# Performance work log

Hardware: AMD Instinct MI355X
Metric: run time of the kernel (lower is better)

Reference implementation:

```python
import jax, jax.numpy as jnp
import numpy as np

DIM = 768
HEADS = 12
HEAD_DIM = DIM // HEADS
SCALE = HEAD_DIM ** -0.5
LN_EPS = 1e-5


def setup_inputs() -> dict:
    key = jax.random.key(0)
    ks = jax.random.split(key, 12)
    B, N, C = 8, 1024, DIM
    g = (6.0 / (C + 3 * C)) ** 0.5  # xavier_uniform bound for qkv
    gp = (6.0 / (C + C)) ** 0.5     # xavier_uniform bound for proj
    return {
        "x": jax.random.normal(ks[0], (B, N, C), jnp.float32),
        "w_qkv_id": jax.random.uniform(ks[1], (3 * C, C), jnp.float32, -g, g),
        "w_qkv_cloth": jax.random.uniform(ks[2], (3 * C, C), jnp.float32, -g, g),
        "w_proj_id": jax.random.uniform(ks[3], (C, C), jnp.float32, -gp, gp),
        "b_proj_id": jnp.zeros((C,), jnp.float32),
        "w_proj_cloth": jax.random.uniform(ks[4], (C, C), jnp.float32, -gp, gp),
        "b_proj_cloth": jnp.zeros((C,), jnp.float32),
        "ln_id_w": jnp.ones((C,), jnp.float32),
        "ln_id_b": jnp.zeros((C,), jnp.float32),
        "ln_cloth_w": jnp.ones((C,), jnp.float32),
        "ln_cloth_b": jnp.zeros((C,), jnp.float32),
        "orth_scale": jnp.asarray(0.1, jnp.float32),
    }


def _layernorm(x, w, b):
    mu = jnp.mean(x, axis=-1, keepdims=True)
    var = jnp.var(x, axis=-1, keepdims=True)
    return (x - mu) * jax.lax.rsqrt(var + LN_EPS) * w + b


def _split_heads(qkv, B, N):
    qkv = qkv.reshape(B, N, 3, HEADS, HEAD_DIM).transpose(2, 0, 3, 1, 4)
    return qkv[0], qkv[1], qkv[2]


def _attn(q, k, v):
    s = jnp.einsum("bhnd,bhmd->bhnm", q, k) * SCALE
    s = jnp.clip(s, -20.0, 20.0)
    a = jax.nn.softmax(s, axis=-1)
    a = jnp.where(jnp.isnan(a), jnp.zeros_like(a), a)  # nan guard (dropout = eval/identity)
    return jnp.einsum("bhnm,bhmd->bhnd", a, v)


def reference(x, w_qkv_id, w_qkv_cloth, w_proj_id, b_proj_id, w_proj_cloth,
              b_proj_cloth, ln_id_w, ln_id_b, ln_cloth_w, ln_cloth_b, orth_scale):
    B, N, C = x.shape
    q_id, k_id, v_id = _split_heads(x @ w_qkv_id.T, B, N)
    q_cl, k_cl, v_cl = _split_heads(x @ w_qkv_cloth.T, B, N)

    # Gram-Schmidt orthogonal projection of q_id against q_cloth
    dot = jnp.sum(q_id * q_cl, axis=-1, keepdims=True)          # [B,H,N,1]
    norm_sq = jnp.sum(q_cl * q_cl, axis=-1, keepdims=True) + 1e-5
    coeff = jnp.clip(dot / norm_sq, -1.0, 1.0)
    scale = jnp.clip(orth_scale, 0.0, 1.0)
    q_id_ortho = q_id - scale * (coeff * q_cl)
    saliency = jnp.clip(jnp.mean(jnp.abs(dot) / jnp.sqrt(norm_sq), axis=1), 0.0, 1.0)  # [B,N,1]

    out_id = _attn(q_id_ortho, k_id, v_id).transpose(0, 2, 1, 3).reshape(B, N, C)
    out_cl = _attn(q_cl, k_cl, v_cl).transpose(0, 2, 1, 3).reshape(B, N, C)

    id_feat = _layernorm(out_id @ w_proj_id.T + b_proj_id, ln_id_w, ln_id_b)
    cl_feat = _layernorm(out_cl @ w_proj_cloth.T + b_proj_cloth, ln_cloth_w, ln_cloth_b)
    return id_feat, cl_feat, saliency
```

## Files before the change

kernel.cpp:

```cpp
#include <hip/hip_runtime.h>

typedef unsigned short u16;
typedef short s16x8 __attribute__((ext_vector_type(8)));
typedef float f32x4 __attribute__((ext_vector_type(4)));

#define DEV __device__ __forceinline__

#if __has_builtin(__builtin_amdgcn_exp2f)
#define EXP2F(x) __builtin_amdgcn_exp2f(x)
#else
#define EXP2F(x) exp2f(x)
#endif

DEV u16 f2bf(float f) {
  unsigned int u = __float_as_uint(f);
  u = (u + 0x7fffu + ((u >> 16) & 1u)) >> 16;
  return (u16)u;
}
DEV float bf2f(u16 h) { return __uint_as_float(((unsigned int)h) << 16); }
DEV unsigned int pk_trunc(float lo, float hi) {
  return __builtin_amdgcn_perm(__float_as_uint(hi), __float_as_uint(lo), 0x07060302u);
}

DEV void g2l16(const void* g, void* l) {
  __builtin_amdgcn_global_load_lds(
      (const __attribute__((address_space(1))) unsigned int*)g,
      (__attribute__((address_space(3))) unsigned int*)l, 16, 0, 0);
}

#define SPLANE 6291456

__global__ __launch_bounds__(256) void k_cvt(const float* __restrict__ x,
                                             const float* __restrict__ wqi,
                                             const float* __restrict__ wqc,
                                             const float* __restrict__ wpi,
                                             const float* __restrict__ wpc,
                                             u16* __restrict__ xb,
                                             u16* __restrict__ wqkv,
                                             u16* __restrict__ wproj) {
  int i = blockIdx.x * 256 + threadIdx.x;
  const float* src; u16* dst; int off;
  if (i < 1572864)      { src = x;   dst = xb;             off = 0; }
  else if (i < 2015232) { src = wqi; dst = wqkv;           off = 1572864; }
  else if (i < 2457600) { src = wqc; dst = wqkv + 1769472; off = 2015232; }
  else if (i < 2605056) { src = wpi; dst = wproj;          off = 2457600; }
  else                  { src = wpc; dst = wproj + 589824; off = 2605056; }
  int j = i - off;
  float4 v = ((const float4*)src)[j];
  ushort4 o;
  o.x = f2bf(v.x); o.y = f2bf(v.y); o.z = f2bf(v.z); o.w = f2bf(v.w);
  ((ushort4*)dst)[j] = o;
}

__global__ __launch_bounds__(256) void k_qkv_gemm(const u16* __restrict__ X,
                                                  const u16* __restrict__ Wq,
                                                  u16* __restrict__ QK,
                                                  u16* __restrict__ VT) {
  __shared__ __align__(16) u16 sm[18432];
  u16* lA = sm;
  u16* lB = sm + 8192;
  const int z = blockIdx.z;
  const int n0 = blockIdx.x * 128, m0 = blockIdx.y * 128;
  const u16* W = Wq + (size_t)z * 2304 * 768;
  const int tid = threadIdx.x;
  const int wave = tid >> 6, lane = tid & 63;
  const int wr = (wave >> 1) * 64, wc = (wave & 1) * 64;
  const int fr = lane & 15, fq = lane >> 4;

  f32x4 acc[4][4];
#pragma unroll
  for (int i = 0; i < 4; i++)
#pragma unroll
    for (int j = 0; j < 4; j++) acc[i][j] = (f32x4){0.f, 0.f, 0.f, 0.f};

  const int srow = lane >> 3;
  const int scol = ((lane & 7) ^ srow) * 8;

  for (int k0 = 0; k0 < 768; k0 += 64) {
    __syncthreads();
#pragma unroll
    for (int it = 0; it < 4; ++it) {
      int rb = wave * 32 + it * 8;
      g2l16(X + (size_t)(m0 + rb + srow) * 768 + k0 + scol, &lA[rb * 64]);
      g2l16(W + (size_t)(n0 + rb + srow) * 768 + k0 + scol, &lB[rb * 64]);
    }
    __syncthreads();
#pragma unroll
    for (int ks = 0; ks < 2; ++ks) {
      s16x8 af[4], bfr[4];
#pragma unroll
      for (int i = 0; i < 4; i++) {
        int row = wc + i * 16 + fr;
        af[i] = *(const s16x8*)&lB[row * 64 + (((ks * 4 + fq) ^ (row & 7)) * 8)];
      }
#pragma unroll
      for (int j = 0; j < 4; j++) {
        int row = wr + j * 16 + fr;
        bfr[j] = *(const s16x8*)&lA[row * 64 + (((ks * 4 + fq) ^ (row & 7)) * 8)];
      }
#pragma unroll
      for (int i = 0; i < 4; i++)
#pragma unroll
        for (int j = 0; j < 4; j++)
          acc[i][j] = __builtin_amdgcn_mfma_f32_16x16x32_bf16(af[i], bfr[j], acc[i][j], 0, 0, 0);
    }
  }

  __syncthreads();
  u16* ep = sm + wave * 4608;
#pragma unroll
  for (int i = 0; i < 4; i++)
#pragma unroll
    for (int j = 0; j < 4; j++) {
      unsigned int lo = (unsigned int)f2bf(acc[i][j][0]) | ((unsigned int)f2bf(acc[i][j][1]) << 16);
      unsigned int hi = (unsigned int)f2bf(acc[i][j][2]) | ((unsigned int)f2bf(acc[i][j][3]) << 16);
      uint2 pk; pk.x = lo; pk.y = hi;
      *(uint2*)&ep[(j * 16 + fr) * 72 + i * 16 + fq * 4] = pk;
    }
  __builtin_amdgcn_s_waitcnt(0);

  const int c0 = n0 + wc;
  const int t0 = m0 + wr;
  const int b = t0 >> 10, tt0 = t0 & 1023;
  if (c0 < 1536) {
    const int three = (c0 >= 768) ? 1 : 0;
    const int h = (c0 - three * 768) >> 6;
    u16* dst = QK + ((size_t)z * 2 + three) * SPLANE +
               ((size_t)(b * 12 + h) * 1024 + tt0) * 64;
#pragma unroll
    for (int pass = 0; pass < 8; ++pass) {
      int row = pass * 8 + (lane >> 3);
      int dch = (lane & 7) * 8;
      *(uint4*)&dst[(size_t)row * 64 + dch] = *(const uint4*)&ep[row * 72 + dch];
    }
  } else {
    const int h = (c0 - 1536) >> 6;
    u16* dst = VT + (size_t)z * SPLANE + ((size_t)(b * 12 + h) * 64) * 1024 + tt0;
#pragma unroll
    for (int pass = 0; pass < 8; ++pass) {
      int d = pass * 8 + (lane >> 3);
      int tch = (lane & 7) * 8;
      unsigned int w0[4];
#pragma unroll
      for (int k2 = 0; k2 < 4; k2++) {
        unsigned int lo = ep[(tch + k2 * 2) * 72 + d];
        unsigned int hi = ep[(tch + k2 * 2 + 1) * 72 + d];
        w0[k2] = lo | (hi << 16);
      }
      uint4 val;
      val.x = w0[0]; val.y = w0[1]; val.z = w0[2]; val.w = w0[3];
      *(uint4*)&dst[(size_t)d * 1024 + tch] = val;
    }
  }
}

__global__ __launch_bounds__(256) void k_ortho(u16* __restrict__ QK,
                                               const float* __restrict__ orth_scale,
                                               float* __restrict__ sal) {
  const int wave = threadIdx.x >> 6, lane = threadIdx.x & 63;
  const int row = blockIdx.x * 4 + wave;
  const int b = row >> 10, n = row & 1023;
  const float scale = fminf(fmaxf(orth_scale[0], 0.f), 1.f);
  u16* qid = QK;
  u16* qcl = QK + (size_t)2 * SPLANE;
  float sacc = 0.f;
  for (int h = 0; h < 12; ++h) {
    size_t off = (((size_t)(b * 12 + h)) * 1024 + n) * 64 + lane;
    float qi = bf2f(qid[off]);
    float qc = bf2f(qcl[off]);
    float d = qi * qc, nq = qc * qc;
#pragma unroll
    for (int s = 1; s < 64; s <<= 1) { d += __shfl_xor(d, s); nq += __shfl_xor(nq, s); }
    nq += 1e-5f;
    float coeff = fminf(fmaxf(d / nq, -1.f), 1.f);
    qid[off] = f2bf(qi - scale * coeff * qc);
    sacc += fabsf(d) / sqrtf(nq);
  }
  if (lane == 0) sal[row] = fminf(fmaxf(sacc * (1.f / 12.f), 0.f), 1.f);
}

#define AST 72
#define PST 40
__global__ __launch_bounds__(256, 3) void k_attn(const u16* __restrict__ QK,
                                                 const u16* __restrict__ VT,
                                                 u16* __restrict__ aout) {
  __shared__ __align__(16) u16 sm[19456];
  u16* lK = sm;
  u16* lVT = sm + 4608;
  const int z = blockIdx.z, bh = blockIdx.y;
  const int q0 = blockIdx.x * 256;
  const int b = bh / 12, hd = bh - b * 12;
  const size_t plane = (size_t)bh * 65536;
  const u16* Q  = QK + (size_t)z * 2 * SPLANE + plane;
  const u16* K  = QK + ((size_t)z * 2 + 1) * SPLANE + plane;
  const u16* Vt = VT + (size_t)z * SPLANE + plane;

  const int tid = threadIdx.x, wave = tid >> 6, lane = tid & 63;
  const int fr = lane & 15, fq = lane >> 4;
  u16* lP = sm + 9216 + wave * 2560;

  s16x8 qf[4][2];
#pragma unroll
  for (int s = 0; s < 4; s++) {
    const u16* qrow = Q + (size_t)(q0 + wave * 64 + s * 16 + fr) * 64;
    qf[s][0] = *(const s16x8*)&qrow[fq * 8];
    qf[s][1] = *(const s16x8*)&qrow[32 + fq * 8];
  }

  f32x4 oacc[4][4];
  float lsum[4];
#pragma unroll
  for (int s = 0; s < 4; s++) {
    lsum[s] = 0.f;
#pragma unroll
    for (int j = 0; j < 4; j++) oacc[s][j] = (f32x4){0.f, 0.f, 0.f, 0.f};
  }

  const int srow = tid >> 3, sc8 = (tid & 7) * 8;

  uint4 rk0 = *(const uint4*)&K[(size_t)srow * 64 + sc8];
  uint4 rk1 = *(const uint4*)&K[(size_t)(srow + 32) * 64 + sc8];
  uint4 rv0 = *(const uint4*)&Vt[(size_t)srow * 1024 + sc8];
  uint4 rv1 = *(const uint4*)&Vt[(size_t)(srow + 32) * 1024 + sc8];

  for (int kv0 = 0; kv0 < 1024; kv0 += 64) {
    __syncthreads();
    *(uint4*)&lK[srow * AST + sc8]         = rk0;
    *(uint4*)&lK[(srow + 32) * AST + sc8]  = rk1;
    *(uint4*)&lVT[srow * AST + sc8]        = rv0;
    *(uint4*)&lVT[(srow + 32) * AST + sc8] = rv1;
    __syncthreads();

    {
      int nxt = (kv0 + 64) & 1023;
      const u16* kb = K + (size_t)nxt * 64;
      rk0 = *(const uint4*)&kb[(size_t)srow * 64 + sc8];
      rk1 = *(const uint4*)&kb[(size_t)(srow + 32) * 64 + sc8];
      const u16* vb = Vt + nxt;
      rv0 = *(const uint4*)&vb[(size_t)srow * 1024 + sc8];
      rv1 = *(const uint4*)&vb[(size_t)(srow + 32) * 1024 + sc8];
    }

#pragma unroll
    for (int ph = 0; ph < 2; ++ph) {
#pragma unroll
      for (int jh = 0; jh < 2; ++jh) {
        const int jt = ph * 2 + jh;
        s16x8 kf0 = *(const s16x8*)&lK[(jt * 16 + fr) * AST + fq * 8];
        s16x8 kf1 = *(const s16x8*)&lK[(jt * 16 + fr) * AST + 32 + fq * 8];
#pragma unroll
        for (int s = 0; s < 4; s++) {
          f32x4 t = (f32x4){0.f, 0.f, 0.f, 0.f};
          t = __builtin_amdgcn_mfma_f32_16x16x32_bf16(kf0, qf[s][0], t, 0, 0, 0);
          t = __builtin_amdgcn_mfma_f32_16x16x32_bf16(kf1, qf[s][1], t, 0, 0, 0);
          float p0 = EXP2F(fmaf(t[0], 0.18033688f, -28.8539008f));
          float p1 = EXP2F(fmaf(t[1], 0.18033688f, -28.8539008f));
          float p2 = EXP2F(fmaf(t[2], 0.18033688f, -28.8539008f));
          float p3 = EXP2F(fmaf(t[3], 0.18033688f, -28.8539008f));
          lsum[s] += (p0 + p1) + (p2 + p3);
          uint2 pk; pk.x = pk_trunc(p0, p1); pk.y = pk_trunc(p2, p3);
          *(uint2*)&lP[(s * 16 + fr) * PST + jh * 16 + fq * 4] = pk;
        }
      }
      __builtin_amdgcn_s_waitcnt(0);
      s16x8 pa[4];
#pragma unroll
      for (int s = 0; s < 4; s++) pa[s] = *(const s16x8*)&lP[(s * 16 + fr) * PST + fq * 8];
#pragma unroll
      for (int jt = 0; jt < 4; jt++) {
        s16x8 vb = *(const s16x8*)&lVT[(jt * 16 + fr) * AST + ph * 32 + fq * 8];
#pragma unroll
        for (int s = 0; s < 4; s++)
          oacc[s][jt] = __builtin_amdgcn_mfma_f32_16x16x32_bf16(pa[s], vb, oacc[s][jt], 0, 0, 0);
      }
    }
  }

#pragma unroll
  for (int s = 0; s < 4; s++) {
    float v = lsum[s];
    v += __shfl_xor(v, 16);
    v += __shfl_xor(v, 32);
    lsum[s] = v;
  }
#pragma unroll
  for (int s = 0; s < 4; s++) {
#pragma unroll
    for (int r = 0; r < 4; r++) {
      float inv = 1.f / __shfl(lsum[s], fq * 4 + r);
      int t = q0 + wave * 64 + s * 16 + fq * 4 + r;
      size_t base = ((size_t)z * 8192 + b * 1024 + t) * 768 + hd * 64 + fr;
#pragma unroll
      for (int jt = 0; jt < 4; jt++)
        aout[base + jt * 16] = f2bf(oacc[s][jt][r] * inv);
    }
  }
}

__global__ __launch_bounds__(256) void k_proj_gemm(const u16* __restrict__ A,
                                                   const u16* __restrict__ Wp,
                                                   const float* __restrict__ bias_id,
                                                   const float* __restrict__ bias_cl,
                                                   u16* __restrict__ out) {
  __shared__ __align__(16) u16 sm[18432];
  u16* lA = sm;
  u16* lB = sm + 8192;
  const int z = blockIdx.z;
  const int n0 = blockIdx.x * 128, m0 = blockIdx.y * 128;
  const u16* Az = A + (size_t)z * 8192 * 768;
  const u16* Wz = Wp + (size_t)z * 768 * 768;
  const float* bias = z ? bias_cl : bias_id;
  u16* oz = out + (size_t)z * 8192 * 768;
  const int tid = threadIdx.x;
  const int wave = tid >> 6, lane = tid & 63;
  const int wr = (wave >> 1) * 64, wc = (wave & 1) * 64;
  const int fr = lane & 15, fq = lane >> 4;

  float bv[4][4];
#pragma unroll
  for (int i = 0; i < 4; i++)
#pragma unroll
    for (int r = 0; r < 4; r++) bv[i][r] = bias[n0 + wc + i * 16 + fq * 4 + r];

  f32x4 acc[4][4];
#pragma unroll
  for (int i = 0; i < 4; i++)
#pragma unroll
    for (int j = 0; j < 4; j++) acc[i][j] = (f32x4){0.f, 0.f, 0.f, 0.f};

  const int srow = lane >> 3;
  const int scol = ((lane & 7) ^ srow) * 8;

  for (int k0 = 0; k0 < 768; k0 += 64) {
    __syncthreads();
#pragma unroll
    for (int it = 0; it < 4; ++it) {
      int rb = wave * 32 + it * 8;
      g2l16(Az + (size_t)(m0 + rb + srow) * 768 + k0 + scol, &lA[rb * 64]);
      g2l16(Wz + (size_t)(n0 + rb + srow) * 768 + k0 + scol, &lB[rb * 64]);
    }
    __syncthreads();
#pragma unroll
    for (int ks = 0; ks < 2; ++ks) {
      s16x8 af[4], bfr[4];
#pragma unroll
      for (int i = 0; i < 4; i++) {
        int row = wc + i * 16 + fr;
        af[i] = *(const s16x8*)&lB[row * 64 + (((ks * 4 + fq) ^ (row & 7)) * 8)];
      }
#pragma unroll
      for (int j = 0; j < 4; j++) {
        int row = wr + j * 16 + fr;
        bfr[j] = *(const s16x8*)&lA[row * 64 + (((ks * 4 + fq) ^ (row & 7)) * 8)];
      }
#pragma unroll
      for (int i = 0; i < 4; i++)
#pragma unroll
        for (int j = 0; j < 4; j++)
          acc[i][j] = __builtin_amdgcn_mfma_f32_16x16x32_bf16(af[i], bfr[j], acc[i][j], 0, 0, 0);
    }
  }

  __syncthreads();
  u16* ep = sm + wave * 4608;
#pragma unroll
  for (int i = 0; i < 4; i++)
#pragma unroll
    for (int j = 0; j < 4; j++) {
      unsigned int lo = (unsigned int)f2bf(acc[i][j][0] + bv[i][0]) |
                        ((unsigned int)f2bf(acc[i][j][1] + bv[i][1]) << 16);
      unsigned int hi = (unsigned int)f2bf(acc[i][j][2] + bv[i][2]) |
                        ((unsigned int)f2bf(acc[i][j][3] + bv[i][3]) << 16);
      uint2 pk; pk.x = lo; pk.y = hi;
      *(uint2*)&ep[(j * 16 + fr) * 72 + i * 16 + fq * 4] = pk;
    }
  __builtin_amdgcn_s_waitcnt(0);

  const int c0 = n0 + wc;
#pragma unroll
  for (int pass = 0; pass < 8; ++pass) {
    int row = pass * 8 + (lane >> 3);
    int dch = (lane & 7) * 8;
    u16* dst = oz + (size_t)(m0 + wr + row) * 768 + c0;
    *(uint4*)&dst[dch] = *(const uint4*)&ep[row * 72 + dch];
  }
}

__global__ __launch_bounds__(256) void k_ln(const u16* __restrict__ pin,
                                            const float* __restrict__ w_id,
                                            const float* __restrict__ b_id,
                                            const float* __restrict__ w_cl,
                                            const float* __restrict__ b_cl,
                                            float* __restrict__ out) {
  __shared__ float red[2][8];
  const int row = blockIdx.x;
  const int z = row >> 13;
  const float* w = z ? w_cl : w_id;
  const float* bb = z ? b_cl : b_id;
  const u16* x = pin + (size_t)row * 768;
  float v[3];
  float s = 0.f, s2 = 0.f;
#pragma unroll
  for (int i = 0; i < 3; i++) {
    v[i] = bf2f(x[threadIdx.x + i * 256]);
    s += v[i];
    s2 += v[i] * v[i];
  }
#pragma unroll
  for (int sh = 1; sh < 64; sh <<= 1) { s += __shfl_xor(s, sh); s2 += __shfl_xor(s2, sh); }
  const int wave = threadIdx.x >> 6, lane = threadIdx.x & 63;
  if (lane == 0) { red[0][wave] = s; red[1][wave] = s2; }
  __syncthreads();
  s = red[0][0] + red[0][1] + red[0][2] + red[0][3];
  s2 = red[1][0] + red[1][1] + red[1][2] + red[1][3];
  float mu = s * (1.f / 768.f);
  float var = s2 * (1.f / 768.f) - mu * mu;
  float rstd = rsqrtf(fmaxf(var, 0.f) + 1e-5f);
  float* o = out + (size_t)row * 768;
#pragma unroll
  for (int i = 0; i < 3; i++) {
    int c = threadIdx.x + i * 256;
    o[c] = (v[i] - mu) * rstd * w[c] + bb[c];
  }
}

extern "C" void kernel_launch(void* const* d_in, const int* in_sizes, int n_in,
                              void* d_out, int out_size, void* d_ws, size_t ws_size,
                              hipStream_t stream) {
  const float* x        = (const float*)d_in[0];
  const float* w_qkv_id = (const float*)d_in[1];
  const float* w_qkv_cl = (const float*)d_in[2];
  const float* w_proj_id= (const float*)d_in[3];
  const float* b_proj_id= (const float*)d_in[4];
  const float* w_proj_cl= (const float*)d_in[5];
  const float* b_proj_cl= (const float*)d_in[6];
  const float* ln_id_w  = (const float*)d_in[7];
  const float* ln_id_b  = (const float*)d_in[8];
  const float* ln_cl_w  = (const float*)d_in[9];
  const float* ln_cl_b  = (const float*)d_in[10];
  const float* orth     = (const float*)d_in[11];
  float* out = (float*)d_out;

  u16* xb    = (u16*)d_ws;
  u16* wqkv  = xb + 6291456;
  u16* wproj = wqkv + 3538944;
  u16* qk    = wproj + 1179648;
  u16* vt    = qk + 25165824;
  u16* aout  = vt + 12582912;
  u16* pout  = qk;

  k_cvt<<<10752, 256, 0, stream>>>(x, w_qkv_id, w_qkv_cl, w_proj_id, w_proj_cl,
                                   xb, wqkv, wproj);
  k_qkv_gemm<<<dim3(18, 64, 2), 256, 0, stream>>>(xb, wqkv, qk, vt);
  k_ortho<<<2048, 256, 0, stream>>>(qk, orth, out + 12582912);
  k_attn<<<dim3(4, 96, 2), 256, 0, stream>>>(qk, vt, aout);
  k_proj_gemm<<<dim3(6, 64, 2), 256, 0, stream>>>(aout, wproj, b_proj_id, b_proj_cl, pout);
  k_ln<<<16384, 256, 0, stream>>>(pout, ln_id_w, ln_id_b, ln_cl_w, ln_cl_b, out);
}
```

Before: 323.4 us.

## Rewrite QKV GEMM as 256x256 double-buffered pipelined kernel with block swizzle

Replaces the 128x128, 4-wave QKV GEMM with a 256x256-tile, 8-wave kernel that double-buffers LDS and interleaves global-to-LDS slab loads with MFMA quarters under explicit barriers, vmcnt waits and priority bumps. A 1D grid with an XCD-aware swizzle improves L2 reuse across blocks. The intent is to overlap memory traffic with matrix compute and raise arithmetic intensity per block. It uses 128KB of LDS and more registers, and the hand-tuned wait counts and barriers are fragile.

```diff
diff --git a/kernel.cpp b/kernel.cpp
--- a/kernel.cpp
+++ b/kernel.cpp
@@ -52,105 +52,189 @@
   ((ushort4*)dst)[j] = o;
 }
 
-__global__ __launch_bounds__(256) void k_qkv_gemm(const u16* __restrict__ X,
-                                                  const u16* __restrict__ Wq,
-                                                  u16* __restrict__ QK,
-                                                  u16* __restrict__ VT) {
-  __shared__ __align__(16) u16 sm[18432];
-  u16* lA = sm;
-  u16* lB = sm + 8192;
-  const int z = blockIdx.z;
-  const int n0 = blockIdx.x * 128, m0 = blockIdx.y * 128;
-  const u16* W = Wq + (size_t)z * 2304 * 768;
+
+#define BAR __builtin_amdgcn_s_barrier()
+#define WAIT_LGKM0 asm volatile("s_waitcnt lgkmcnt(0)" ::: "memory")
+#define WAIT_VM(n) asm volatile("s_waitcnt vmcnt(" #n ")" ::: "memory")
+#define PRIO1 __builtin_amdgcn_s_setprio(1)
+#define PRIO0 __builtin_amdgcn_s_setprio(0)
+
+#define SLAB(gbase, rowoff, kt, ldst) \
+  g2l16((gbase) + (size_t)((rowoff) + wrow) * 768 + (kt) * 64 + csrc, (ldst) + wave * 512)
+
+template<int I0>
+DEV void ldA2(s16x8 (&dst)[2][2], const u16* bw, int aOff, int c0, int c1) {
+#pragma unroll
+  for (int i = 0; i < 2; i++) {
+    dst[i][0] = *(const s16x8*)&bw[aOff + (I0 + i) * 1024 + c0];
+    dst[i][1] = *(const s16x8*)&bw[aOff + (I0 + i) * 1024 + c1];
+  }
+}
+template<int J0>
+DEV void ldB4(s16x8 (&dst)[4][2], const u16* bx, int bOff, int c0, int c1) {
+#pragma unroll
+  for (int j = 0; j < 4; j++) {
+    dst[j][0] = *(const s16x8*)&bx[bOff + (J0 + j) * 1024 + c0];
+    dst[j][1] = *(const s16x8*)&bx[bOff + (J0 + j) * 1024 + c1];
+  }
+}
+template<int I0, int J0>
+DEV void mmq(const s16x8 (&af)[2][2], const s16x8 (&bf)[4][2], f32x4 (&acc)[4][8]) {
+#pragma unroll
+  for (int ks = 0; ks < 2; ks++)
+#pragma unroll
+    for (int i = 0; i < 2; i++)
+#pragma unroll
+      for (int j = 0; j < 4; j++)
+        acc[I0 + i][J0 + j] = __builtin_amdgcn_mfma_f32_16x16x32_bf16(
+            af[i][ks], bf[j][ks], acc[I0 + i][J0 + j], 0, 0, 0);
+}
+
+__global__ __launch_bounds__(512, 2) void k_qkv_gemm(const u16* __restrict__ X,
+                                                     const u16* __restrict__ Wq,
+                                                     u16* __restrict__ QK,
+                                                     u16* __restrict__ VT) {
+  __shared__ __align__(16) u16 sm[65536];
+
+  const int idx = blockIdx.x;
+  const int swz = (idx & 7) * 72 + (idx >> 3);
+  const int bx = swz % 9;
+  const int tmp = swz / 9;
+  const int by = tmp & 31;
+  const int z = tmp >> 5;
+  const int n0 = bx * 256, m0 = by * 256;
+
   const int tid = threadIdx.x;
   const int wave = tid >> 6, lane = tid & 63;
-  const int wr = (wave >> 1) * 64, wc = (wave & 1) * 64;
+  const int wr = wave >> 2, wc = wave & 3;
   const int fr = lane & 15, fq = lane >> 4;
 
-  f32x4 acc[4][4];
+  const int r8 = lane >> 3;
+  const int csrc = ((lane & 7) ^ r8) * 8;
+  const int wrow = wave * 8 + r8;
+
+  const int c0 = (fq ^ (fr & 7)) * 8;
+  const int c1 = ((fq + 4) ^ (fr & 7)) * 8;
+  const int aOff = (wc * 64 + fr) * 64;
+  const int bOff = (wr * 128 + fr) * 64;
+
+  const u16* GA = Wq + (size_t)z * (2304 * 768) + (size_t)n0 * 768;
+  const u16* GB = X + (size_t)m0 * 768;
+
+  u16* const lw0 = sm;
+  u16* const lx0 = sm + 16384;
+  u16* const lw1 = sm + 32768;
+  u16* const lx1 = sm + 49152;
+
+  f32x4 acc[4][8];
 #pragma unroll
   for (int i = 0; i < 4; i++)
 #pragma unroll
-    for (int j = 0; j < 4; j++) acc[i][j] = (f32x4){0.f, 0.f, 0.f, 0.f};
-
-  const int srow = lane >> 3;
-  const int scol = ((lane & 7) ^ srow) * 8;
-
-  for (int k0 = 0; k0 < 768; k0 += 64) {
-    __syncthreads();
-#pragma unroll
-    for (int it = 0; it < 4; ++it) {
-      int rb = wave * 32 + it * 8;
-      g2l16(X + (size_t)(m0 + rb + srow) * 768 + k0 + scol, &lA[rb * 64]);
-      g2l16(W + (size_t)(n0 + rb + srow) * 768 + k0 + scol, &lB[rb * 64]);
-    }
-    __syncthreads();
-#pragma unroll
-    for (int ks = 0; ks < 2; ++ks) {
-      s16x8 af[4], bfr[4];
-#pragma unroll
-      for (int i = 0; i < 4; i++) {
-        int row = wc + i * 16 + fr;
-        af[i] = *(const s16x8*)&lB[row * 64 + (((ks * 4 + fq) ^ (row & 7)) * 8)];
-      }
-#pragma unroll
-      for (int j = 0; j < 4; j++) {
-        int row = wr + j * 16 + fr;
-        bfr[j] = *(const s16x8*)&lA[row * 64 + (((ks * 4 + fq) ^ (row & 7)) * 8)];
-      }
-#pragma unroll
-      for (int i = 0; i < 4; i++)
-#pragma unroll
-        for (int j = 0; j < 4; j++)
-          acc[i][j] = __builtin_amdgcn_mfma_f32_16x16x32_bf16(af[i], bfr[j], acc[i][j], 0, 0, 0);
-    }
+    for (int j = 0; j < 8; j++) acc[i][j] = (f32x4){0.f, 0.f, 0.f, 0.f};
+
+  SLAB(GA,   0, 0, lw0);
+  SLAB(GA,  64, 0, lw0 + 4096);
+  SLAB(GA, 128, 0, lw0 + 8192);
+  SLAB(GA, 192, 0, lw0 + 12288);
+  SLAB(GB,   0, 0, lx0);
+  SLAB(GB,  64, 0, lx0 + 4096);
+  SLAB(GB, 128, 0, lx0 + 8192);
+  SLAB(GB, 192, 0, lx0 + 12288);
+  SLAB(GA,   0, 1, lw1);
+  SLAB(GA,  64, 1, lw1 + 4096);
+  WAIT_VM(2);
+  BAR;
+
+  s16x8 afA[2][2], afB[2][2], bfA[4][2], bfB[4][2];
+
+#pragma unroll
+  for (int it = 0; it < 6; ++it) {
+    const int ktB = 2 * it + 1;
+    const int ktN = 2 * it + 2;
+    const int ktM = 2 * it + 3;
+    const bool last = (it == 5);
+
+    ldA2<0>(afA, lw0, aOff, c0, c1);
+    ldB4<0>(bfA, lx0, bOff, c0, c1);
+    SLAB(GA, 128, ktB, lw1 + 8192);
+    SLAB(GA, 192, ktB, lw1 + 12288);
+    BAR; WAIT_LGKM0; PRIO1; mmq<0, 0>(afA, bfA, acc); PRIO0; BAR;
+    ldB4<4>(bfB, lx0, bOff, c0, c1);
+    SLAB(GB,   0, ktB, lx1);
+    SLAB(GB,  64, ktB, lx1 + 4096);
+    BAR; WAIT_LGKM0; PRIO1; mmq<0, 4>(afA, bfB, acc); PRIO0; BAR;
+    ldA2<2>(afB, lw0, aOff, c0, c1);
+    SLAB(GB, 128, ktB, lx1 + 8192);
+    SLAB(GB, 192, ktB, lx1 + 12288);
+    BAR; WAIT_LGKM0; PRIO1; mmq<2, 4>(afB, bfB, acc); PRIO0; BAR;
+    if (!last) { SLAB(GA, 0, ktN, lw0); SLAB(GA, 64, ktN, lw0 + 4096); }
+    BAR; PRIO1; mmq<2, 0>(afB, bfA, acc); PRIO0;
+    if (!last) { WAIT_VM(2); } else { WAIT_VM(0); }
+    BAR;
+    ldA2<0>(afA, lw1, aOff, c0, c1);
+    ldB4<0>(bfA, lx1, bOff, c0, c1);
+    if (!last) { SLAB(GA, 128, ktN, lw0 + 8192); SLAB(GA, 192, ktN, lw0 + 12288); }
+    BAR; WAIT_LGKM0; PRIO1; mmq<0, 0>(afA, bfA, acc); PRIO0; BAR;
+    ldB4<4>(bfB, lx1, bOff, c0, c1);
+    if (!last) { SLAB(GB, 0, ktN, lx0); SLAB(GB, 64, ktN, lx0 + 4096); }
+    BAR; WAIT_LGKM0; PRIO1; mmq<0, 4>(afA, bfB, acc); PRIO0; BAR;
+    ldA2<2>(afB, lw1, aOff, c0, c1);
+    if (!last) { SLAB(GB, 128, ktN, lx0 + 8192); SLAB(GB, 192, ktN, lx0 + 12288); }
+    BAR; WAIT_LGKM0; PRIO1; mmq<2, 4>(afB, bfB, acc); PRIO0; BAR;
+    if (!last) { SLAB(GA, 0, ktM, lw1); SLAB(GA, 64, ktM, lw1 + 4096); }
+    BAR; PRIO1; mmq<2, 0>(afB, bfA, acc); PRIO0;
+    if (!last) WAIT_VM(2);
+    BAR;
   }
 
   __syncthreads();
   u16* ep = sm + wave * 4608;
-#pragma unroll
-  for (int i = 0; i < 4; i++)
-#pragma unroll
-    for (int j = 0; j < 4; j++) {
-      unsigned int lo = (unsigned int)f2bf(acc[i][j][0]) | ((unsigned int)f2bf(acc[i][j][1]) << 16);
-      unsigned int hi = (unsigned int)f2bf(acc[i][j][2]) | ((unsigned int)f2bf(acc[i][j][3]) << 16);
-      uint2 pk; pk.x = lo; pk.y = hi;
-      *(uint2*)&ep[(j * 16 + fr) * 72 + i * 16 + fq * 4] = pk;
-    }
-  __builtin_amdgcn_s_waitcnt(0);
-
-  const int c0 = n0 + wc;
-  const int t0 = m0 + wr;
-  const int b = t0 >> 10, tt0 = t0 & 1023;
-  if (c0 < 1536) {
-    const int three = (c0 >= 768) ? 1 : 0;
-    const int h = (c0 - three * 768) >> 6;
-    u16* dst = QK + ((size_t)z * 2 + three) * SPLANE +
-               ((size_t)(b * 12 + h) * 1024 + tt0) * 64;
-#pragma unroll
-    for (int pass = 0; pass < 8; ++pass) {
-      int row = pass * 8 + (lane >> 3);
-      int dch = (lane & 7) * 8;
-      *(uint4*)&dst[(size_t)row * 64 + dch] = *(const uint4*)&ep[row * 72 + dch];
-    }
-  } else {
-    const int h = (c0 - 1536) >> 6;
-    u16* dst = VT + (size_t)z * SPLANE + ((size_t)(b * 12 + h) * 64) * 1024 + tt0;
-#pragma unroll
-    for (int pass = 0; pass < 8; ++pass) {
-      int d = pass * 8 + (lane >> 3);
-      int tch = (lane & 7) * 8;
-      unsigned int w0[4];
-#pragma unroll
-      for (int k2 = 0; k2 < 4; k2++) {
-        unsigned int lo = ep[(tch + k2 * 2) * 72 + d];
-        unsigned int hi = ep[(tch + k2 * 2 + 1) * 72 + d];
-        w0[k2] = lo | (hi << 16);
-      }
-      uint4 val;
-      val.x = w0[0]; val.y = w0[1]; val.z = w0[2]; val.w = w0[3];
-      *(uint4*)&dst[(size_t)d * 1024 + tch] = val;
-    }
+  const int c0h = n0 + wc * 64;
+  const int three = (c0h >= 1536) ? 2 : ((c0h >= 768) ? 1 : 0);
+  const int hh = (c0h - three * 768) >> 6;
+#pragma unroll
+  for (int jp = 0; jp < 2; ++jp) {
+#pragma unroll
+    for (int i = 0; i < 4; i++)
+#pragma unroll
+      for (int j4 = 0; j4 < 4; j4++) {
+        const int j = jp * 4 + j4;
+        uint2 pk;
+        pk.x = (unsigned int)f2bf(acc[i][j][0]) | ((unsigned int)f2bf(acc[i][j][1]) << 16);
+        pk.y = (unsigned int)f2bf(acc[i][j][2]) | ((unsigned int)f2bf(acc[i][j][3]) << 16);
+        *(uint2*)&ep[(j4 * 16 + fr) * 72 + i * 16 + fq * 4] = pk;
+      }
+    WAIT_LGKM0;
+    const int trow0 = m0 + wr * 128 + jp * 64;
+    const int b = trow0 >> 10, tt0 = trow0 & 1023;
+    if (three < 2) {
+      u16* dst = QK + ((size_t)z * 2 + three) * SPLANE +
+                 ((size_t)(b * 12 + hh) * 1024 + tt0) * 64;
+#pragma unroll
+      for (int pass = 0; pass < 8; ++pass) {
+        int row = pass * 8 + (lane >> 3);
+        int dch = (lane & 7) * 8;
+        *(uint4*)&dst[(size_t)row * 64 + dch] = *(const uint4*)&ep[row * 72 + dch];
+      }
+    } else {
+      u16* dst = VT + (size_t)z * SPLANE + ((size_t)(b * 12 + hh) * 64) * 1024 + tt0;
+#pragma unroll
+      for (int pass = 0; pass < 8; ++pass) {
+        int d = pass * 8 + (lane >> 3);
+        int tch = (lane & 7) * 8;
+        unsigned int w0[4];
+#pragma unroll
+        for (int k2 = 0; k2 < 4; k2++) {
+          unsigned int lo = ep[(tch + k2 * 2) * 72 + d];
+          unsigned int hi = ep[(tch + k2 * 2 + 1) * 72 + d];
+          w0[k2] = lo | (hi << 16);
+        }
+        uint4 val;
+        val.x = w0[0]; val.y = w0[1]; val.z = w0[2]; val.w = w0[3];
+        *(uint4*)&dst[(size_t)d * 1024 + tch] = val;
+      }
+    }
+    if (jp == 0) WAIT_LGKM0;
   }
 }
 
@@ -451,7 +535,7 @@
 
   k_cvt<<<10752, 256, 0, stream>>>(x, w_qkv_id, w_qkv_cl, w_proj_id, w_proj_cl,
                                    xb, wqkv, wproj);
-  k_qkv_gemm<<<dim3(18, 64, 2), 256, 0, stream>>>(xb, wqkv, qk, vt);
+  k_qkv_gemm<<<576, 512, 0, stream>>>(xb, wqkv, qk, vt);
   k_ortho<<<2048, 256, 0, stream>>>(qk, orth, out + 12582912);
   k_attn<<<dim3(4, 96, 2), 256, 0, stream>>>(qk, vt, aout);
   k_proj_gemm<<<dim3(6, 64, 2), 256, 0, stream>>>(aout, wproj, b_proj_id, b_proj_cl, pout);
```

After: 347.8 us. 1.08x slower.

## Double-buffer QKV GEMM LDS staging with vmcnt waits and block swizzle

Applied to the files above, without the earlier changes.

Restructures the QKV projection GEMM main loop to use two LDS buffers, so the global-to-LDS loads for the next K slice run while MFMAs consume the current one. Partial vmcnt waits and raw barriers replace the full syncthreads pairs. It also remaps a 1D grid with an XCD-style swizzle so neighbouring tiles share L2, and raises MFMA issue priority during compute. LDS use doubles to 64KB per block and launch bounds request 2 blocks per CU, which may limit occupancy.

```diff
diff --git a/kernel.cpp b/kernel.cpp
--- a/kernel.cpp
+++ b/kernel.cpp
@@ -29,6 +29,11 @@
 }
 
 #define SPLANE 6291456
+
+#define BAR __builtin_amdgcn_s_barrier()
+#define WAIT_VM(n) asm volatile("s_waitcnt vmcnt(" #n ")" ::: "memory")
+#define PRIO1 __builtin_amdgcn_s_setprio(1)
+#define PRIO0 __builtin_amdgcn_s_setprio(0)
 
 __global__ __launch_bounds__(256) void k_cvt(const float* __restrict__ x,
                                              const float* __restrict__ wqi,
@@ -52,58 +57,104 @@
   ((ushort4*)dst)[j] = o;
 }
 
-__global__ __launch_bounds__(256) void k_qkv_gemm(const u16* __restrict__ X,
-                                                  const u16* __restrict__ Wq,
-                                                  u16* __restrict__ QK,
-                                                  u16* __restrict__ VT) {
-  __shared__ __align__(16) u16 sm[18432];
-  u16* lA = sm;
-  u16* lB = sm + 8192;
-  const int z = blockIdx.z;
-  const int n0 = blockIdx.x * 128, m0 = blockIdx.y * 128;
-  const u16* W = Wq + (size_t)z * 2304 * 768;
+
+DEV void qstg(const u16* pX, const u16* pW, int koff, u16* lA, u16* lB, int wave) {
+#pragma unroll
+  for (int it = 0; it < 4; ++it) {
+    int rb = wave * 32 + it * 8;
+    g2l16(pX + koff + it * (8 * 768), &lA[rb * 64]);
+    g2l16(pW + koff + it * (8 * 768), &lB[rb * 64]);
+  }
+}
+
+DEV void qcomp(const u16* lA, const u16* lB, int wr, int wc, int fr, int fq,
+               f32x4 (&acc)[4][4]) {
+#pragma unroll
+  for (int ks = 0; ks < 2; ++ks) {
+    s16x8 af[4], bfr[4];
+#pragma unroll
+    for (int i = 0; i < 4; i++) {
+      int row = wc + i * 16 + fr;
+      af[i] = *(const s16x8*)&lB[row * 64 + (((ks * 4 + fq) ^ (row & 7)) * 8)];
+    }
+#pragma unroll
+    for (int j = 0; j < 4; j++) {
+      int row = wr + j * 16 + fr;
+      bfr[j] = *(const s16x8*)&lA[row * 64 + (((ks * 4 + fq) ^ (row & 7)) * 8)];
+    }
+    PRIO1;
+#pragma unroll
+    for (int i = 0; i < 4; i++)
+#pragma unroll
+      for (int j = 0; j < 4; j++)
+        acc[i][j] = __builtin_amdgcn_mfma_f32_16x16x32_bf16(af[i], bfr[j], acc[i][j], 0, 0, 0);
+    PRIO0;
+  }
+}
+
+__global__ __launch_bounds__(256, 2) void k_qkv_gemm(const u16* __restrict__ X,
+                                                     const u16* __restrict__ Wq,
+                                                     u16* __restrict__ QK,
+                                                     u16* __restrict__ VT) {
+  __shared__ __align__(16) u16 sm[32768];
+
+  const int idx = blockIdx.x;
+  const int swz = (idx & 7) * 288 + (idx >> 3);
+  const int bx = swz % 18;
+  const int rem = swz / 18;
+  const int by = rem & 63;
+  const int z = rem >> 6;
+  const int n0 = bx * 128, m0 = by * 128;
+
   const int tid = threadIdx.x;
   const int wave = tid >> 6, lane = tid & 63;
   const int wr = (wave >> 1) * 64, wc = (wave & 1) * 64;
   const int fr = lane & 15, fq = lane >> 4;
 
-  f32x4 acc[4][4];
-#pragma unroll
-  for (int i = 0; i < 4; i++)
-#pragma unroll
-    for (int j = 0; j < 4; j++) acc[i][j] = (f32x4){0.f, 0.f, 0.f, 0.f};
-
   const int srow = lane >> 3;
   const int scol = ((lane & 7) ^ srow) * 8;
 
-  for (int k0 = 0; k0 < 768; k0 += 64) {
-    __syncthreads();
-#pragma unroll
-    for (int it = 0; it < 4; ++it) {
-      int rb = wave * 32 + it * 8;
-      g2l16(X + (size_t)(m0 + rb + srow) * 768 + k0 + scol, &lA[rb * 64]);
-      g2l16(W + (size_t)(n0 + rb + srow) * 768 + k0 + scol, &lB[rb * 64]);
-    }
-    __syncthreads();
-#pragma unroll
-    for (int ks = 0; ks < 2; ++ks) {
-      s16x8 af[4], bfr[4];
-#pragma unroll
-      for (int i = 0; i < 4; i++) {
-        int row = wc + i * 16 + fr;
-        af[i] = *(const s16x8*)&lB[row * 64 + (((ks * 4 + fq) ^ (row & 7)) * 8)];
-      }
-#pragma unroll
-      for (int j = 0; j < 4; j++) {
-        int row = wr + j * 16 + fr;
-        bfr[j] = *(const s16x8*)&lA[row * 64 + (((ks * 4 + fq) ^ (row & 7)) * 8)];
-      }
-#pragma unroll
-      for (int i = 0; i < 4; i++)
-#pragma unroll
-        for (int j = 0; j < 4; j++)
-          acc[i][j] = __builtin_amdgcn_mfma_f32_16x16x32_bf16(af[i], bfr[j], acc[i][j], 0, 0, 0);
-    }
+  const u16* pX = X + (size_t)(m0 + wave * 32 + srow) * 768 + scol;
+  const u16* pW = Wq + (size_t)z * (2304 * 768) + (size_t)(n0 + wave * 32 + srow) * 768 + scol;
+
+  u16* const lA0 = sm;
+  u16* const lB0 = sm + 8192;
+  u16* const lA1 = sm + 16384;
+  u16* const lB1 = sm + 24576;
+
+  f32x4 acc[4][4];
+#pragma unroll
+  for (int i = 0; i < 4; i++)
+#pragma unroll
+    for (int j = 0; j < 4; j++) acc[i][j] = (f32x4){0.f, 0.f, 0.f, 0.f};
+
+  qstg(pX, pW, 0, lA0, lB0, wave);
+  qstg(pX, pW, 64, lA1, lB1, wave);
+  WAIT_VM(8);
+  BAR;
+
+  const u16* pX2 = pX + 128;
+  const u16* pW2 = pW + 128;
+
+#pragma unroll
+  for (int ii = 0; ii < 6; ++ii) {
+    qcomp(lA0, lB0, wr, wc, fr, fq, acc);
+    BAR;
+    if (ii < 5) {
+      qstg(pX2, pW2, 0, lA0, lB0, wave);
+      WAIT_VM(8);
+    } else {
+      WAIT_VM(0);
+    }
+    BAR;
+    qcomp(lA1, lB1, wr, wc, fr, fq, acc);
+    BAR;
+    if (ii < 5) {
+      qstg(pX2, pW2, 64, lA1, lB1, wave);
+      WAIT_VM(8);
+      pX2 += 128; pW2 += 128;
+    }
+    BAR;
   }
 
   __syncthreads();
@@ -451,7 +502,7 @@
 
   k_cvt<<<10752, 256, 0, stream>>>(x, w_qkv_id, w_qkv_cl, w_proj_id, w_proj_cl,
                                    xb, wqkv, wproj);
-  k_qkv_gemm<<<dim3(18, 64, 2), 256, 0, stream>>>(xb, wqkv, qk, vt);
+  k_qkv_gemm<<<2304, 256, 0, stream>>>(xb, wqkv, qk, vt);
   k_ortho<<<2048, 256, 0, stream>>>(qk, orth, out + 12582912);
   k_attn<<<dim3(4, 96, 2), 256, 0, stream>>>(qk, vt, aout);
   k_proj_gemm<<<dim3(6, 64, 2), 256, 0, stream>>>(aout, wproj, b_proj_id, b_proj_cl, pout);
```

Result: faster. 312.6 us (-3.3%).
